# Optimization experiments

Hardware: AMD Instinct MI355X
Metric: run time of the kernel (lower is better)

The kernel has to match this reference:

```python
import jax, jax.numpy as jnp
import numpy as np

THRESHOLD = 0.5     # overlap_thresh
NEG_POS = 3         # negative:positive ratio
VAR = (0.1, 0.2)    # cfg['variance']


def point_form(pr):
    # cxcywh -> xmin,ymin,xmax,ymax
    return jnp.concatenate([pr[:, :2] - pr[:, 2:] / 2, pr[:, :2] + pr[:, 2:] / 2], axis=1)


def jaccard(a, b):
    # a: [N,4] point-form truths, b: [P,4] point-form priors -> IoU [N,P]
    lt = jnp.maximum(a[:, None, :2], b[None, :, :2])
    rb = jnp.minimum(a[:, None, 2:], b[None, :, 2:])
    wh = jnp.clip(rb - lt, 0.0)
    inter = wh[..., 0] * wh[..., 1]
    area_a = ((a[:, 2] - a[:, 0]) * (a[:, 3] - a[:, 1]))[:, None]
    area_b = ((b[:, 2] - b[:, 0]) * (b[:, 3] - b[:, 1]))[None, :]
    return inter / (area_a + area_b - inter)


def encode(matched, priors):
    # matched: [P,4] point-form, priors: [P,4] cxcywh
    g_cxcy = ((matched[:, :2] + matched[:, 2:]) / 2 - priors[:, :2]) / (VAR[0] * priors[:, 2:])
    g_wh = jnp.log((matched[:, 2:] - matched[:, :2]) / priors[:, 2:]) / VAR[1]
    return jnp.concatenate([g_cxcy, g_wh], axis=1)


def match_one(truths, labels, priors):
    # truths [N,4], labels [N], priors [P,4] cxcywh
    N = truths.shape[0]
    P = priors.shape[0]
    overlaps = jaccard(truths, point_form(priors))          # [N,P]
    best_prior_idx = jnp.argmax(overlaps, axis=1)           # [N] best prior per truth
    best_truth_overlap = jnp.max(overlaps, axis=0)          # [P]
    best_truth_idx = jnp.argmax(overlaps, axis=0)           # [P]
    # ensure each truth's best prior is kept (overlap forced to 2)
    best_truth_overlap = best_truth_overlap.at[best_prior_idx].set(2.0)
    hit = best_prior_idx[:, None] == jnp.arange(P)[None, :]  # [N,P]
    chosen = jnp.max(jnp.where(hit, jnp.arange(N)[:, None], -1), axis=0)
    best_truth_idx = jnp.where(chosen >= 0, chosen, best_truth_idx)
    matched = truths[best_truth_idx]                        # [P,4]
    conf = labels[best_truth_idx].astype(jnp.int32) + 1
    conf = jnp.where(best_truth_overlap < THRESHOLD, 0, conf)
    return encode(matched, priors), conf


def smooth_l1(x):
    ax = jnp.abs(x)
    return jnp.where(ax < 1.0, 0.5 * ax * ax, ax - 0.5)


def multibox_loss(loc_data, conf_data, priors, targets):
    num, P, C = conf_data.shape
    truths = targets[..., :4]
    labels = targets[..., 4]
    loc_t, conf_t = jax.vmap(match_one, in_axes=(0, 0, None))(truths, labels, priors)
    pos = conf_t > 0                                        # [B,P]

    # localization loss over positives
    loss_l = jnp.sum(jnp.where(pos[..., None], smooth_l1(loc_data - loc_t), 0.0))

    # hard-negative mining score: logsumexp - conf[label clamped to {0,1}]
    batch_conf = jax.lax.stop_gradient(conf_data).reshape(-1, C)
    conf_flat = conf_t.reshape(-1)
    clamped = jnp.where(conf_flat != 0, 1, conf_flat)
    # replicate torch nonzero()-indexing quirk: row 0 also set to 1 if any positive exists
    clamped = clamped.at[0].set(jnp.where(jnp.any(conf_flat != 0), 1, clamped[0]))
    lse = jax.scipy.special.logsumexp(batch_conf, axis=1)
    loss_c = lse - jnp.take_along_axis(batch_conf, clamped[:, None], axis=1)[:, 0]
    loss_c = loss_c.reshape(num, P)
    loss_c = jnp.where(pos, 0.0, loss_c)
    # rank of each prior by descending mining loss
    idx_rank = jnp.argsort(jnp.argsort(-loss_c, axis=1), axis=1)
    num_pos = jnp.sum(pos.astype(jnp.int32), axis=1, keepdims=True)  # [B,1]
    num_neg = jnp.clip(NEG_POS * num_pos, None, P - 1)
    neg = idx_rank < num_neg
    sel = pos | neg

    # confidence cross-entropy over selected priors, original labels as targets
    logp = jax.nn.log_softmax(conf_data, axis=-1)           # [B,P,C]
    ce = -jnp.take_along_axis(logp, conf_t[..., None], axis=-1)[..., 0]
    loss_conf = jnp.sum(jnp.where(sel, ce, 0.0))

    Nf = jnp.sum(num_pos).astype(jnp.float32)
    return loss_l / Nf, loss_conf / Nf


def setup_inputs() -> dict:
    key = jax.random.key(0)
    k1, k2, k3, k4, k5, k6, k7 = jax.random.split(key, 7)
    B, P, C, NOBJ = 128, 8732, 21, 20
    loc_data = jax.random.normal(k1, (B, P, 4), jnp.float32)
    conf_data = jax.random.normal(k2, (B, P, C), jnp.float32)
    pcxy = jax.random.uniform(k3, (P, 2), jnp.float32, 0.05, 0.95)
    pwh = jax.random.uniform(k4, (P, 2), jnp.float32, 0.05, 0.4)
    priors = jnp.concatenate([pcxy, pwh], axis=1)           # cxcywh
    mins = jax.random.uniform(k5, (B, NOBJ, 2), jnp.float32, 0.0, 0.6)
    wh = jax.random.uniform(k6, (B, NOBJ, 2), jnp.float32, 0.05, 0.35)
    lab = jax.random.randint(k7, (B, NOBJ), 0, C - 1).astype(jnp.float32)
    targets = jnp.concatenate([mins, mins + wh, lab[..., None]], axis=-1)
    return {"loc_data": loc_data, "conf_data": conf_data, "priors": priors, "targets": targets}


def reference(loc_data, conf_data, priors, targets):
    return multibox_loss(loc_data, conf_data, priors, targets)
```

## Files before the change

### kernel.cpp

```cpp
#include <hip/hip_runtime.h>

#define PP 8732
#define NB 20
#define NC 21
#define BTH 256
#define NCH 9
#define BTS 1024
#define NWS (BTS/64)

__device__ __forceinline__ float sl1(float d){
  float a = fabsf(d);
  return a < 1.0f ? 0.5f*a*a : a - 0.5f;
}

__device__ __forceinline__ float wave_max64(float x){
  int t;
  t = __builtin_amdgcn_update_dpp(0, __float_as_int(x), 0x111, 0xF, 0xF, true); x = fmaxf(x, __int_as_float(t));
  t = __builtin_amdgcn_update_dpp(0, __float_as_int(x), 0x112, 0xF, 0xF, true); x = fmaxf(x, __int_as_float(t));
  t = __builtin_amdgcn_update_dpp(0, __float_as_int(x), 0x114, 0xF, 0xF, true); x = fmaxf(x, __int_as_float(t));
  t = __builtin_amdgcn_update_dpp(0, __float_as_int(x), 0x118, 0xF, 0xF, true); x = fmaxf(x, __int_as_float(t));
  t = __builtin_amdgcn_update_dpp(0, __float_as_int(x), 0x142, 0xF, 0xF, true); x = fmaxf(x, __int_as_float(t));
  t = __builtin_amdgcn_update_dpp(0, __float_as_int(x), 0x143, 0xF, 0xF, true); x = fmaxf(x, __int_as_float(t));
  return __int_as_float(__builtin_amdgcn_readlane(__float_as_int(x), 63));
}

__device__ __forceinline__ int wave_sum64_lane63(int x){
  x += __builtin_amdgcn_update_dpp(0, x, 0x111, 0xF, 0xF, true);
  x += __builtin_amdgcn_update_dpp(0, x, 0x112, 0xF, 0xF, true);
  x += __builtin_amdgcn_update_dpp(0, x, 0x114, 0xF, 0xF, true);
  x += __builtin_amdgcn_update_dpp(0, x, 0x118, 0xF, 0xF, true);
  x += __builtin_amdgcn_update_dpp(0, x, 0x142, 0xF, 0xF, true);
  x += __builtin_amdgcn_update_dpp(0, x, 0x143, 0xF, 0xF, true);
  return x;
}

extern "C" __global__ void __launch_bounds__(BTH)
mb_main(const float* __restrict__ conf_data,
        const float* __restrict__ priors,
        const float* __restrict__ targets,
        float* __restrict__ rankneg,
        unsigned char* __restrict__ meta,
        unsigned long long* __restrict__ keys2)
{
  const int b = blockIdx.x, chunk = blockIdx.y;
  const int tid = threadIdx.x, lane = tid & 63, wid = tid >> 6;
  const int q0w = chunk*1024 + wid*256;
  const int p0  = q0w + 4*lane;

  __shared__ float4 s_tr4[NB];
  __shared__ float  s_area[NB];
  __shared__ unsigned long long s_keys[4][NB];

  if (tid < NB){
    const float* tp = targets + ((long)b*NB + tid)*5;
    float a0=tp[0], a1=tp[1], a2=tp[2], a3=tp[3];
    s_tr4[tid]  = make_float4(a0,a1,a2,a3);
    s_area[tid] = (a2-a0)*(a3-a1);
  }
  __syncthreads();

  unsigned long long mykey = 0ULL;

  if (q0w < PP){
    const bool fullwave = (q0w + 256 <= PP);

    float bx1[4], by1[4], bx2[4], by2[4], areab[4];
    #pragma unroll
    for (int i=0;i<4;i++){
      int p = p0 + i;
      int pc = (p < PP) ? p : 0;
      float4 pr = reinterpret_cast<const float4*>(priors)[pc];
      float x1 = pr.x - pr.z*0.5f, y1 = pr.y - pr.w*0.5f;
      float x2 = pr.x + pr.z*0.5f, y2 = pr.y + pr.w*0.5f;
      if (!fullwave && p >= PP){ x1=3e9f; y1=3e9f; x2=3e9f; y2=3e9f; }
      bx1[i]=x1; by1[i]=y1; bx2[i]=x2; by2[i]=y2;
      areab[i] = (x2-x1)*(y2-y1);
    }

    float bestov[4] = {-1.f,-1.f,-1.f,-1.f};
    int   bestn [4] = {0,0,0,0};

    #pragma unroll 4
    for (int n=0;n<NB;n++){
      float4 t = s_tr4[n];
      float aa = s_area[n];
      float candiou = -1.0f; unsigned candp = 0u;
      #pragma unroll
      for (int i=0;i<4;i++){
        float lx=fmaxf(t.x,bx1[i]), ly=fmaxf(t.y,by1[i]);
        float rx=fminf(t.z,bx2[i]), ry=fminf(t.w,by2[i]);
        float iw=fmaxf(rx-lx,0.f), ih=fmaxf(ry-ly,0.f);
        float inter = iw*ih;
        float iou = inter * __builtin_amdgcn_rcpf(aa + areab[i] - inter);
        if (iou > bestov[i]){ bestov[i]=iou; bestn[i]=n; }
        if (iou > candiou){ candiou=iou; candp=(unsigned)(p0+i); }
      }
      float wmax = wave_max64(candiou);
      unsigned long long mk = __ballot(candiou == wmax);
      int wlane = __ffsll((long long)mk) - 1;
      unsigned wp = (unsigned)__builtin_amdgcn_readlane((int)candp, wlane);
      unsigned long long key = ((unsigned long long)__float_as_uint(wmax)<<32)
                             | (unsigned long long)(0xFFFFFFFFu - wp);
      if (lane == n) mykey = key;
    }

    float rr4[4] = {0.f,0.f,0.f,0.f};
    unsigned metab = 0u;
    #pragma unroll
    for (int i=0;i<4;i++){
      int p = p0 + i;
      if (p < PP){
        const float* cb = conf_data + ((long)b*PP + p)*NC;
        const float4* cb4 = reinterpret_cast<const float4*>(cb);
        float4 ca0=cb4[0], ca1=cb4[1], ca2=cb4[2], ca3=cb4[3], ca4=cb4[4];
        float c20 = cb[20];
        float vv[NC] = {ca0.x,ca0.y,ca0.z,ca0.w, ca1.x,ca1.y,ca1.z,ca1.w,
                        ca2.x,ca2.y,ca2.z,ca2.w, ca3.x,ca3.y,ca3.z,ca3.w,
                        ca4.x,ca4.y,ca4.z,ca4.w, c20};
        float m = vv[0];
        #pragma unroll
        for (int c=1;c<NC;c++) m = fmaxf(m, vv[c]);
        float s = 0.f;
        #pragma unroll
        for (int c=0;c<NC;c++) s += __expf(vv[c]-m);
        float lse = __logf(s) + m;
        rr4[i] = lse - vv[0];
        metab |= ((unsigned)((bestn[i]<<1) | (bestov[i] >= 0.5f ? 1 : 0))) << (8*i);
      }
    }

    if (p0 + 3 < PP){
      *reinterpret_cast<float4*>(rankneg + (long)b*PP + p0) =
          make_float4(rr4[0],rr4[1],rr4[2],rr4[3]);
      *reinterpret_cast<unsigned*>(meta + (long)b*PP + p0) = metab;
    } else {
      #pragma unroll
      for (int i=0;i<4;i++){
        int p = p0 + i;
        if (p < PP){
          rankneg[(long)b*PP + p] = rr4[i];
          meta[(long)b*PP + p] = (unsigned char)((metab >> (8*i)) & 0xFF);
        }
      }
    }
  }

  if (lane < NB) s_keys[wid][lane] = mykey;
  __syncthreads();
  if (tid < NB){
    unsigned long long mx = s_keys[0][tid];
    #pragma unroll
    for (int w=1;w<4;w++) if (s_keys[w][tid] > mx) mx = s_keys[w][tid];
    keys2[((long)b*NCH + chunk)*NB + tid] = mx;
  }
}

extern "C" __global__ void __launch_bounds__(BTS)
mb_select(const float* __restrict__ loc_data,
          const float* __restrict__ conf_data,
          const float* __restrict__ priors,
          const float* __restrict__ targets,
          const float* __restrict__ rankneg,
          const unsigned char* __restrict__ meta,
          const unsigned long long* __restrict__ keys2,
          float* __restrict__ rowres, int* __restrict__ ticket,
          float* __restrict__ out, int Bn)
{
  const int b = blockIdx.x, tid = threadIdx.x, lane = tid & 63, wid = tid >> 6;
  __shared__ __align__(16) float s_val[PP];
  __shared__ __align__(16) unsigned int s_meta4[PP/4];
  __shared__ float4 s_tr4[NB];
  __shared__ float s_lab[NB];
  __shared__ int   s_bp[NB];
  __shared__ int   s_tot[32];
  __shared__ float s_fa[NWS], s_fb[NWS], s_fc[NWS];
  __shared__ int   s_ia[NWS];
  __shared__ float s_rowll, s_rowpc;
  __shared__ int   s_npos, s_last;
  unsigned char* s_meta = (unsigned char*)s_meta4;
  float4* sv4 = reinterpret_cast<float4*>(s_val);

  const float4* rr = reinterpret_cast<const float4*>(rankneg + (long)b*PP);
  for (int i=tid;i<PP/4;i+=BTS) sv4[i]=rr[i];
  const unsigned int* mr = reinterpret_cast<const unsigned int*>(meta + (long)b*PP);
  for (int i=tid;i<PP/4;i+=BTS) s_meta4[i]=mr[i];
  if (tid < NB*5){
    int n = tid/5, k2 = tid-n*5;
    float vv = targets[((long)b*NB+n)*5+k2];
    if (k2<4) ((float*)&s_tr4[n])[k2]=vv; else s_lab[n]=vv;
  }
  if (tid < NB){
    unsigned long long mx = 0ULL;
    #pragma unroll
    for (int c=0;c<NCH;c++){
      unsigned long long kk = keys2[((long)b*NCH + c)*NB + tid];
      if (kk > mx) mx = kk;
    }
    s_bp[tid] = (int)(0xFFFFFFFFu - (unsigned)(mx & 0xFFFFFFFFULL));
  }
  if (tid < 32) s_tot[tid] = 0;
  __syncthreads();

  if (tid==0){
    for (int n=0;n<NB;n++) s_meta[s_bp[n]] = (unsigned char)((n<<1)|1);
  }
  __syncthreads();

  float4 rv0 = sv4[tid];
  float4 rv1 = sv4[tid+1024];
  float4 rv2 = (tid < PP/4-2048) ? sv4[tid+2048] : make_float4(0.f,0.f,0.f,0.f);
  unsigned mm0 = s_meta4[tid];
  unsigned mm1 = s_meta4[tid+1024];
  unsigned mm2 = (tid < PP/4-2048) ? s_meta4[tid+2048] : 0u;
  if (mm0 & 0x00000001u) rv0.x = 0.f;
  if (mm0 & 0x00000100u) rv0.y = 0.f;
  if (mm0 & 0x00010000u) rv0.z = 0.f;
  if (mm0 & 0x01000000u) rv0.w = 0.f;
  if (mm1 & 0x00000001u) rv1.x = 0.f;
  if (mm1 & 0x00000100u) rv1.y = 0.f;
  if (mm1 & 0x00010000u) rv1.z = 0.f;
  if (mm1 & 0x01000000u) rv1.w = 0.f;
  if (mm2 & 0x00000001u) rv2.x = 0.f;
  if (mm2 & 0x00000100u) rv2.y = 0.f;
  if (mm2 & 0x00010000u) rv2.z = 0.f;
  if (mm2 & 0x01000000u) rv2.w = 0.f;

  int spec = 0; float delta = 0.f, val0 = 0.f;
  if (b==0 && tid==0 && !(mm0 & 1u)){
    float v0 = conf_data[0], v1 = conf_data[1];
    float r0 = rv0.x;
    float r0p = r0 + v0 - v1;
    delta = r0 - r0p;
    spec = 1;
    rv0.x = r0p; val0 = r0p;
  }

  float ll=0.f, pc=0.f; int np=0;
  for (int p=tid;p<PP;p+=BTS){
    int mt = s_meta[p];
    if (mt & 1){
      np++;
      int n = mt>>1;
      int ct = (int)s_lab[n] + 1;
      const float* cp = conf_data + ((long)b*PP+p)*NC;
      float v0 = cp[0], vct = cp[ct];
      pc += s_val[p] + v0 - vct;
      float4 t = s_tr4[n];
      float4 prr = reinterpret_cast<const float4*>(priors)[p];
      float4 ld = reinterpret_cast<const float4*>(loc_data)[(long)b*PP+p];
      float g0 = ((t.x+t.z)*0.5f - prr.x)/(0.1f*prr.z);
      float g1 = ((t.y+t.w)*0.5f - prr.y)/(0.1f*prr.w);
      float g2 = __logf((t.z-t.x)/prr.z)/0.2f;
      float g3 = __logf((t.w-t.y)/prr.w)/0.2f;
      ll += sl1(ld.x-g0)+sl1(ld.y-g1)+sl1(ld.z-g2)+sl1(ld.w-g3);
    }
  }
  #pragma unroll
  for (int o=32;o;o>>=1){
    ll += __shfl_down(ll,o,64);
    pc += __shfl_down(pc,o,64);
    np += __shfl_down(np,o,64);
  }
  if (lane==0){ s_fa[wid]=ll; s_fb[wid]=pc; s_ia[wid]=np; }
  __syncthreads();
  if (tid==0){
    float a=0.f,c2=0.f; int ni=0;
    for (int w=0;w<NWS;w++){ a+=s_fa[w]; c2+=s_fb[w]; ni+=s_ia[w]; }
    s_rowll=a; s_rowpc=c2; s_npos=ni;
  }
  __syncthreads();
  const int num_pos = s_npos;
  int k = num_pos*3; if (k > PP-1) k = PP-1;

  float negsum = 0.f;
  if (k > 0){
    unsigned lo=0u, hi=0x7f800000u;
    int it=0;
    while (lo < hi){
      unsigned mid = lo + ((hi - lo + 1u) >> 1);
      int c = (__float_as_uint(rv0.x)>=mid) + (__float_as_uint(rv0.y)>=mid)
            + (__float_as_uint(rv0.z)>=mid) + (__float_as_uint(rv0.w)>=mid)
            + (__float_as_uint(rv1.x)>=mid) + (__float_as_uint(rv1.y)>=mid)
            + (__float_as_uint(rv1.z)>=mid) + (__float_as_uint(rv1.w)>=mid)
            + (__float_as_uint(rv2.x)>=mid) + (__float_as_uint(rv2.y)>=mid)
            + (__float_as_uint(rv2.z)>=mid) + (__float_as_uint(rv2.w)>=mid);
      c = wave_sum64_lane63(c);
      if (lane==63) atomicAdd(&s_tot[it], c);
      __syncthreads();
      int tot = s_tot[it];
      if (tot >= k) lo = mid; else hi = mid - 1u;
      it++;
    }
    const unsigned vstar = lo;

    int cg=0; float sg=0.f;
    #define ACC(x) if (__float_as_uint(x)>vstar){cg++;sg+=(x);}
    ACC(rv0.x) ACC(rv0.y) ACC(rv0.z) ACC(rv0.w)
    ACC(rv1.x) ACC(rv1.y) ACC(rv1.z) ACC(rv1.w)
    ACC(rv2.x) ACC(rv2.y) ACC(rv2.z) ACC(rv2.w)
    #undef ACC
    #pragma unroll
    for (int o=32;o;o>>=1){ cg += __shfl_down(cg,o,64); sg += __shfl_down(sg,o,64); }
    __syncthreads();
    if (lane==0){ s_ia[wid]=cg; s_fa[wid]=sg; }
    __syncthreads();
    if (tid==0){
      int cG=0; float sumG=0.f;
      for (int w=0;w<NWS;w++){ cG+=s_ia[w]; sumG+=s_fa[w]; }
      int tie = k - cG;
      negsum = sumG + (float)tie * __uint_as_float(vstar);
      if (b==0 && spec && __float_as_uint(val0) >= vstar) negsum += delta;
    }
  }

  if (tid==0){
    rowres[b*4+0] = s_rowll;
    rowres[b*4+1] = s_rowpc + negsum;
    rowres[b*4+2] = (float)num_pos;
    __threadfence();
    int t = atomicAdd(ticket, 1);
    s_last = (t == Bn - 1) ? 1 : 0;
  }
  __syncthreads();

  if (s_last){
    __threadfence();
    float a0=0.f, a1=0.f, a2=0.f;
    for (int i=tid;i<Bn;i+=BTS){
      a0 += rowres[i*4+0]; a1 += rowres[i*4+1]; a2 += rowres[i*4+2];
    }
    #pragma unroll
    for (int o=32;o;o>>=1){
      a0 += __shfl_down(a0,o,64);
      a1 += __shfl_down(a1,o,64);
      a2 += __shfl_down(a2,o,64);
    }
    if (lane==0){ s_fa[wid]=a0; s_fb[wid]=a1; s_fc[wid]=a2; }
    __syncthreads();
    if (tid==0){
      float A0=0.f,A1=0.f,A2=0.f;
      for (int w=0;w<NWS;w++){ A0+=s_fa[w]; A1+=s_fb[w]; A2+=s_fc[w]; }
      out[0] = A0/A2;
      out[1] = A1/A2;
    }
  }
}

extern "C" void kernel_launch(void* const* d_in, const int* in_sizes, int n_in,
                              void* d_out, int out_size, void* d_ws, size_t ws_size,
                              hipStream_t stream) {
  const float* loc     = (const float*)d_in[0];
  const float* conf    = (const float*)d_in[1];
  const float* priors  = (const float*)d_in[2];
  const float* targets = (const float*)d_in[3];
  float* out = (float*)d_out;
  int B = in_sizes[0] / (PP*4);

  char* ws = (char*)d_ws;
  int*   ticket = (int*)ws;
  float* rowres = (float*)(ws + 64);
  unsigned long long* keys2 = (unsigned long long*)(ws + 4096);
  size_t off_rank = 4096 + (size_t)B*NCH*NB*8;
  float* rankneg = (float*)(ws + off_rank);
  unsigned char* metaa = (unsigned char*)(ws + off_rank + (size_t)B*PP*4);

  hipMemsetAsync(d_ws, 0, 64, stream);
  hipLaunchKernelGGL(mb_main,   dim3(B, NCH), dim3(BTH), 0, stream,
                     conf, priors, targets, rankneg, metaa, keys2);
  hipLaunchKernelGGL(mb_select, dim3(B), dim3(BTS), 0, stream,
                     loc, conf, priors, targets, rankneg, metaa, keys2,
                     rowres, ticket, out, B);
}
```

Baseline: 206.3 us.

## Halve per-thread prior count, double chunks, broadcast truths via readlane

Each thread in mb_main now handles 2 priors instead of 4, with 512-prior chunks and 18 chunks per batch. That doubles the grid and aims to raise occupancy and latency hiding, with a launch-bounds hint of 6 blocks per CU. Truth boxes are held in lane registers and broadcast with readlane, which removes the shared-memory staging and one barrier. The cost is more blocks and twice as many per-chunk key outputs for mb_select to reduce. The workspace offset is also aligned to 256 bytes.

```diff
diff --git a/kernel.cpp b/kernel.cpp
--- a/kernel.cpp
+++ b/kernel.cpp
@@ -4,7 +4,8 @@
 #define NB 20
 #define NC 21
 #define BTH 256
-#define NCH 9
+#define CHP 512
+#define NCH 18
 #define BTS 1024
 #define NWS (BTS/64)
 
@@ -34,7 +35,7 @@
   return x;
 }
 
-extern "C" __global__ void __launch_bounds__(BTH)
+extern "C" __global__ void __launch_bounds__(BTH, 6)
 mb_main(const float* __restrict__ conf_data,
         const float* __restrict__ priors,
         const float* __restrict__ targets,
@@ -44,51 +45,49 @@
 {
   const int b = blockIdx.x, chunk = blockIdx.y;
   const int tid = threadIdx.x, lane = tid & 63, wid = tid >> 6;
-  const int q0w = chunk*1024 + wid*256;
-  const int p0  = q0w + 4*lane;
-
-  __shared__ float4 s_tr4[NB];
-  __shared__ float  s_area[NB];
+  const int q0w = chunk*CHP + wid*128;
+  const int p0  = q0w + 2*lane;
+
   __shared__ unsigned long long s_keys[4][NB];
 
-  if (tid < NB){
-    const float* tp = targets + ((long)b*NB + tid)*5;
-    float a0=tp[0], a1=tp[1], a2=tp[2], a3=tp[3];
-    s_tr4[tid]  = make_float4(a0,a1,a2,a3);
-    s_area[tid] = (a2-a0)*(a3-a1);
-  }
-  __syncthreads();
+  float tx=0.f, ty=0.f, tz=0.f, tw=0.f;
+  if (lane < NB){
+    const float* tp = targets + ((long)b*NB + lane)*5;
+    tx = tp[0]; ty = tp[1]; tz = tp[2]; tw = tp[3];
+  }
+  const float area_a = (tz-tx)*(tw-ty);
 
   unsigned long long mykey = 0ULL;
 
   if (q0w < PP){
-    const bool fullwave = (q0w + 256 <= PP);
-
-    float bx1[4], by1[4], bx2[4], by2[4], areab[4];
-    #pragma unroll
-    for (int i=0;i<4;i++){
+    float bx1[2], by1[2], bx2[2], by2[2], areab[2];
+    #pragma unroll
+    for (int i=0;i<2;i++){
       int p = p0 + i;
       int pc = (p < PP) ? p : 0;
       float4 pr = reinterpret_cast<const float4*>(priors)[pc];
       float x1 = pr.x - pr.z*0.5f, y1 = pr.y - pr.w*0.5f;
       float x2 = pr.x + pr.z*0.5f, y2 = pr.y + pr.w*0.5f;
-      if (!fullwave && p >= PP){ x1=3e9f; y1=3e9f; x2=3e9f; y2=3e9f; }
+      if (p >= PP){ x1=3e9f; y1=3e9f; x2=3e9f; y2=3e9f; }
       bx1[i]=x1; by1[i]=y1; bx2[i]=x2; by2[i]=y2;
       areab[i] = (x2-x1)*(y2-y1);
     }
 
-    float bestov[4] = {-1.f,-1.f,-1.f,-1.f};
-    int   bestn [4] = {0,0,0,0};
-
-    #pragma unroll 4
+    float bestov[2] = {-1.f,-1.f};
+    int   bestn [2] = {0,0};
+
+    #pragma unroll
     for (int n=0;n<NB;n++){
-      float4 t = s_tr4[n];
-      float aa = s_area[n];
+      float t_x = __int_as_float(__builtin_amdgcn_readlane(__float_as_int(tx), n));
+      float t_y = __int_as_float(__builtin_amdgcn_readlane(__float_as_int(ty), n));
+      float t_z = __int_as_float(__builtin_amdgcn_readlane(__float_as_int(tz), n));
+      float t_w = __int_as_float(__builtin_amdgcn_readlane(__float_as_int(tw), n));
+      float aa  = __int_as_float(__builtin_amdgcn_readlane(__float_as_int(area_a), n));
       float candiou = -1.0f; unsigned candp = 0u;
       #pragma unroll
-      for (int i=0;i<4;i++){
-        float lx=fmaxf(t.x,bx1[i]), ly=fmaxf(t.y,by1[i]);
-        float rx=fminf(t.z,bx2[i]), ry=fminf(t.w,by2[i]);
+      for (int i=0;i<2;i++){
+        float lx=fmaxf(t_x,bx1[i]), ly=fmaxf(t_y,by1[i]);
+        float rx=fminf(t_z,bx2[i]), ry=fminf(t_w,by2[i]);
         float iw=fmaxf(rx-lx,0.f), ih=fmaxf(ry-ly,0.f);
         float inter = iw*ih;
         float iou = inter * __builtin_amdgcn_rcpf(aa + areab[i] - inter);
@@ -104,13 +103,12 @@
       if (lane == n) mykey = key;
     }
 
-    float rr4[4] = {0.f,0.f,0.f,0.f};
-    unsigned metab = 0u;
-    #pragma unroll
-    for (int i=0;i<4;i++){
-      int p = p0 + i;
-      if (p < PP){
-        const float* cb = conf_data + ((long)b*PP + p)*NC;
+    if (p0 < PP){
+      float rr2[2];
+      unsigned metab = 0u;
+      #pragma unroll
+      for (int i=0;i<2;i++){
+        const float* cb = conf_data + ((long)b*PP + p0 + i)*NC;
         const float4* cb4 = reinterpret_cast<const float4*>(cb);
         float4 ca0=cb4[0], ca1=cb4[1], ca2=cb4[2], ca3=cb4[3], ca4=cb4[4];
         float c20 = cb[20];
@@ -124,24 +122,12 @@
         #pragma unroll
         for (int c=0;c<NC;c++) s += __expf(vv[c]-m);
         float lse = __logf(s) + m;
-        rr4[i] = lse - vv[0];
+        rr2[i] = lse - vv[0];
         metab |= ((unsigned)((bestn[i]<<1) | (bestov[i] >= 0.5f ? 1 : 0))) << (8*i);
       }
-    }
-
-    if (p0 + 3 < PP){
-      *reinterpret_cast<float4*>(rankneg + (long)b*PP + p0) =
-          make_float4(rr4[0],rr4[1],rr4[2],rr4[3]);
-      *reinterpret_cast<unsigned*>(meta + (long)b*PP + p0) = metab;
-    } else {
-      #pragma unroll
-      for (int i=0;i<4;i++){
-        int p = p0 + i;
-        if (p < PP){
-          rankneg[(long)b*PP + p] = rr4[i];
-          meta[(long)b*PP + p] = (unsigned char)((metab >> (8*i)) & 0xFF);
-        }
-      }
+      *reinterpret_cast<float2*>(rankneg + (long)b*PP + p0) = make_float2(rr2[0], rr2[1]);
+      *reinterpret_cast<unsigned short*>(meta + (long)b*PP + p0) =
+          (unsigned short)(metab & 0xFFFFu);
     }
   }
 
@@ -360,7 +346,7 @@
   int*   ticket = (int*)ws;
   float* rowres = (float*)(ws + 64);
   unsigned long long* keys2 = (unsigned long long*)(ws + 4096);
-  size_t off_rank = 4096 + (size_t)B*NCH*NB*8;
+  size_t off_rank = (4096 + (size_t)B*NCH*NB*8 + 255) & ~(size_t)255;
   float* rankneg = (float*)(ws + off_rank);
   unsigned char* metaa = (unsigned char*)(ws + off_rank + (size_t)B*PP*4);
 
```

Result: faster. 199.4 us (-3.3%).
